# Kernel optimization log

Hardware: AMD Instinct MI355X
Metric: run time of the kernel (lower is better)

Reference implementation:

```python
import jax, jax.numpy as jnp
import numpy as np

N = 50000          # num nodes
E = 1_000_000      # num edges
H = 64             # hidden_dim
IMG, TWT, NUMP, CAT = 512, 768, 16, 8
NCLS, NET = 2, 3   # num_classes, num_edge_types


def setup_inputs() -> dict:
    key = jax.random.key(0)
    ks = jax.random.split(key, 40)
    f32 = jnp.float32
    w = lambda k, s: (jax.random.normal(k, s, f32) * 0.02)
    inp = {
        # forward args
        "image": jax.random.normal(ks[0], (N, IMG), f32),
        "tweets": jax.random.normal(ks[1], (N, TWT), f32),
        "num_prop": jax.random.normal(ks[2], (N, NUMP), f32),
        "category": jax.random.normal(ks[3], (N, CAT), f32),
        "edge_index": jax.random.randint(ks[4], (2, E), 0, N, jnp.int32),
        "edge_type": jax.random.randint(ks[5], (E,), 0, NET, jnp.int32),
        # explicit randomness (replaces randn_like / Bernoulli.sample)
        "eps": jax.random.normal(ks[6], (E, H), f32),
        "u": jax.random.uniform(ks[7], (E,), f32),
        # parameters (stored [in, out]; y = x @ W + b)
        "Wi": w(ks[8], (IMG, H)), "bi": jnp.zeros((H,), f32),
        "Wt": w(ks[9], (TWT, H)), "bt": jnp.zeros((H,), f32),
        "Wn": w(ks[10], (NUMP, H)), "bn": jnp.zeros((H,), f32),
        "Wc": w(ks[11], (CAT, H)), "bc": jnp.zeros((H,), f32),
        "Wf": w(ks[12], (4 * H, H)), "bf": jnp.zeros((H,), f32),
        "Eet": w(ks[13], (NET, 2 * H)),              # edge_type_embed
        "Wmu": w(ks[14], (2 * H, H)), "bmu": jnp.zeros((H,), f32),
        "Wlv": w(ks[15], (2 * H, H)), "blv": jnp.zeros((H,), f32),
        "Wm1": w(ks[16], (2 * H, 64)), "bm1": jnp.zeros((64,), f32),
        "Wm2": w(ks[17], (64, 1)), "bm2": jnp.zeros((1,), f32),
        "Wcls": w(ks[18], (H, NCLS)), "bcls": jnp.zeros((NCLS,), f32),
    }
    return inp


def reference(image, tweets, num_prop, category, edge_index, edge_type, eps, u,
              Wi, bi, Wt, bt, Wn, bn, Wc, bc, Wf, bf, Eet,
              Wmu, bmu, Wlv, blv, Wm1, bm1, Wm2, bm2, Wcls, bcls):
    relu = jax.nn.relu
    # encode_user
    img_f = relu(image @ Wi + bi)
    twt_f = relu(tweets @ Wt + bt)
    num_f = relu(num_prop @ Wn + bn)
    cat_f = relu(category @ Wc + bc)
    node_features = relu(jnp.concatenate([img_f, twt_f, num_f, cat_f], -1) @ Wf + bf)  # [N, H]

    src, dst = edge_index[0], edge_index[1]
    u_i, u_j = node_features[src], node_features[dst]          # [E, H] each
    edge_emb = relu(jnp.concatenate([u_i, u_j], -1) + Eet[edge_type])  # [E, 2H]

    # parameterized_gaussian (z unused downstream, kept for fidelity)
    mu = edge_emb @ Wmu + bmu
    log_var = edge_emb @ Wlv + blv
    z = mu + eps * jnp.exp(0.5 * log_var)

    # edge confidence + Bernoulli sample via inverse-CDF with provided uniforms
    logits_e = (relu(edge_emb @ Wm1 + bm1) @ Wm2 + bm2)[:, 0]  # [E]
    p_ij = jax.nn.sigmoid(logits_e)
    s = (u < p_ij).astype(node_features.dtype)                 # trusted-edge indicator, [E]

    # segment-mean of dst features over trusted edges, grouped by src
    sums = jax.ops.segment_sum(u_j * s[:, None], src, num_segments=N)  # [N, H]
    cnt = jax.ops.segment_sum(s, src, num_segments=N)                  # [N]
    agg = jnp.where(cnt[:, None] > 0, sums / jnp.maximum(cnt, 1.0)[:, None], node_features)

    return agg @ Wcls + bcls  # [N, num_classes]
```

## Files before the change

kernel.cpp:

```cpp
#include <hip/hip_runtime.h>
#include <cstdint>

typedef short short8 __attribute__((ext_vector_type(8)));
typedef float f32x4  __attribute__((ext_vector_type(4)));

__device__ __forceinline__ void split2(float x, short& h, short& l) {
  unsigned u  = __float_as_uint(x);
  unsigned rh = u + 0x7FFFu + ((u >> 16) & 1u);
  h = (short)(rh >> 16);
  float hf = __uint_as_float((rh >> 16) << 16);
  float lf = x - hf;
  unsigned ul = __float_as_uint(lf);
  unsigned rl = ul + 0x7FFFu + ((ul >> 16) & 1u);
  l = (short)(rl >> 16);
}

__device__ __forceinline__ void split4(float4 a, uint2& hp, uint2& lp) {
  unsigned hp0, hp1, lp0, lp1;
  asm("v_cvt_pk_bf16_f32 %0, %1, %2" : "=v"(hp0) : "v"(a.x), "v"(a.y));
  asm("v_cvt_pk_bf16_f32 %0, %1, %2" : "=v"(hp1) : "v"(a.z), "v"(a.w));
  float h0 = __uint_as_float(hp0 << 16);
  float h1 = __uint_as_float(hp0 & 0xFFFF0000u);
  float h2 = __uint_as_float(hp1 << 16);
  float h3 = __uint_as_float(hp1 & 0xFFFF0000u);
  float l0 = a.x - h0, l1 = a.y - h1, l2 = a.z - h2, l3 = a.w - h3;
  asm("v_cvt_pk_bf16_f32 %0, %1, %2" : "=v"(lp0) : "v"(l0), "v"(l1));
  asm("v_cvt_pk_bf16_f32 %0, %1, %2" : "=v"(lp1) : "v"(l2), "v"(l3));
  hp = make_uint2(hp0, hp1);
  lp = make_uint2(lp0, lp1);
}

__global__ __launch_bounds__(256) void init_head(int* __restrict__ head, int N)
{
  const int i = blockIdx.x * 256 + threadIdx.x;
  if (i < N) head[i] = -1;
}

__global__ __launch_bounds__(256) void prep_w(
    const float* __restrict__ Wi, const float* __restrict__ Wt,
    const float* __restrict__ Wn, const float* __restrict__ Wc,
    const float* __restrict__ Wf, const float* __restrict__ Wm1,
    short* __restrict__ hi, short* __restrict__ lo)
{
  int idx = blockIdx.x * 256 + threadIdx.x;
  if (idx >= 1728 * 64) return;
  int kp = idx >> 6, col = idx & 63;
  const float* W; int K, kloc, base;
  if (kp < 512)       { W = Wi;            K = 512; kloc = kp;        base = 0;    }
  else if (kp < 1280) { W = Wt;            K = 768; kloc = kp - 512;  base = 512;  }
  else if (kp < 1312) { W = Wn;            K = 16;  kloc = kp - 1280; base = 1280; }
  else if (kp < 1344) { W = Wc;            K = 8;   kloc = kp - 1312; base = 1312; }
  else if (kp < 1600) { W = Wf;            K = 256; kloc = kp - 1344; base = 1344; }
  else if (kp < 1664) { W = Wm1;           K = 64;  kloc = kp - 1600; base = 1600; }
  else                { W = Wm1 + 64 * 64; K = 64;  kloc = kp - 1664; base = 1664; }
  float x = (kloc < K) ? W[(size_t)kloc * 64 + col] : 0.f;
  short h, l; split2(x, h, l);
  int s = kloc >> 5;
  int addr = ((s * 4 + (col >> 4)) * 64 + ((col & 15) | (((kloc >> 3) & 3) << 4))) * 8 + (kloc & 7);
  size_t o = (size_t)base * 64 + addr;
  hi[o] = h; lo[o] = l;
}

__global__ __launch_bounds__(256) void encoder(
    const float* __restrict__ image, const float* __restrict__ tweets,
    const float* __restrict__ nump, const float* __restrict__ catg,
    const short* __restrict__ Whi, const short* __restrict__ Wlo,
    const float* __restrict__ bi, const float* __restrict__ bt,
    const float* __restrict__ bn, const float* __restrict__ bc,
    const float* __restrict__ bf, float* __restrict__ nf, int M)
{
  __shared__ float hbuf[4][16 * 68 + 4];
  const int tid = threadIdx.x;
  const int m0  = blockIdx.x * 64;
  const int w   = tid >> 6, l = tid & 63;
  const int r   = l & 15;
  const int g   = l >> 4;
  int grow = m0 + w * 16 + r;
  if (grow >= M) grow = M - 1;

  f32x4 acc[4], acc2[4];
#pragma unroll
  for (int n = 0; n < 4; n++) {
    acc[n]  = (f32x4){0.f, 0.f, 0.f, 0.f};
    acc2[n] = (f32x4){0.f, 0.f, 0.f, 0.f};
  }

  auto mfma_step = [&](float4 a0, float4 a1, int wstep, f32x4* ac) {
    uint2 h01, l01, h23, l23;
    split4(a0, h01, l01);
    split4(a1, h23, l23);
    uint4 ahi_u = make_uint4(h01.x, h01.y, h23.x, h23.y);
    uint4 alo_u = make_uint4(l01.x, l01.y, l23.x, l23.y);
    short8 ahi = *reinterpret_cast<short8*>(&ahi_u);
    short8 alo = *reinterpret_cast<short8*>(&alo_u);
#pragma unroll
    for (int n = 0; n < 4; n++) {
      short8 whi = *reinterpret_cast<const short8*>(&Whi[((size_t)(wstep * 4 + n)) * 512 + l * 8]);
      short8 wlo = *reinterpret_cast<const short8*>(&Wlo[((size_t)(wstep * 4 + n)) * 512 + l * 8]);
      ac[n] = __builtin_amdgcn_mfma_f32_16x16x32_bf16(ahi, whi, ac[n], 0, 0, 0);
      ac[n] = __builtin_amdgcn_mfma_f32_16x16x32_bf16(alo, whi, ac[n], 0, 0, 0);
      ac[n] = __builtin_amdgcn_mfma_f32_16x16x32_bf16(ahi, wlo, ac[n], 0, 0, 0);
    }
  };

  auto seg2_phase = [&](int seg, const float* __restrict__ bias) {
    float* hb = hbuf[w];
#pragma unroll
    for (int n = 0; n < 4; n++) {
      const int c  = n * 16 + r;
      const float bb = bias[c];
#pragma unroll
      for (int j = 0; j < 4; j++) {
        const int row = g * 4 + j;
        hb[row * 68 + c] = fmaxf(acc[n][j] + bb, 0.f);
      }
      acc[n] = (f32x4){0.f, 0.f, 0.f, 0.f};
    }
    asm volatile("s_waitcnt lgkmcnt(0)" ::: "memory");
    __builtin_amdgcn_sched_barrier(0);
#pragma unroll
    for (int ks2 = 0; ks2 < 2; ks2++) {
      float4 b0 = *reinterpret_cast<const float4*>(&hb[r * 68 + ks2 * 32 + g * 8]);
      float4 b1 = *reinterpret_cast<const float4*>(&hb[r * 68 + ks2 * 32 + g * 8 + 4]);
      mfma_step(b0, b1, 42 + seg * 2 + ks2, acc2);
    }
  };

#pragma unroll 4
  for (int t = 0; t < 16; t++) {
    const float* ap = image + (size_t)grow * 512 + t * 32 + g * 8;
    float4 a0 = *reinterpret_cast<const float4*>(ap);
    float4 a1 = *reinterpret_cast<const float4*>(ap + 4);
    mfma_step(a0, a1, t, acc);
  }
  seg2_phase(0, bi);

#pragma unroll 4
  for (int t = 0; t < 24; t++) {
    const float* ap = tweets + (size_t)grow * 768 + t * 32 + g * 8;
    float4 a0 = *reinterpret_cast<const float4*>(ap);
    float4 a1 = *reinterpret_cast<const float4*>(ap + 4);
    mfma_step(a0, a1, 16 + t, acc);
  }
  seg2_phase(1, bt);

  {
    float4 a0 = make_float4(0.f, 0.f, 0.f, 0.f);
    float4 a1 = make_float4(0.f, 0.f, 0.f, 0.f);
    if (g < 2) {
      const float* ap = nump + (size_t)grow * 16 + g * 8;
      a0 = *reinterpret_cast<const float4*>(ap);
      a1 = *reinterpret_cast<const float4*>(ap + 4);
    }
    mfma_step(a0, a1, 40, acc);
  }
  seg2_phase(2, bn);

  {
    float4 a0 = make_float4(0.f, 0.f, 0.f, 0.f);
    float4 a1 = make_float4(0.f, 0.f, 0.f, 0.f);
    if (g == 0) {
      const float* ap = catg + (size_t)grow * 8;
      a0 = *reinterpret_cast<const float4*>(ap);
      a1 = *reinterpret_cast<const float4*>(ap + 4);
    }
    mfma_step(a0, a1, 41, acc);
  }
  seg2_phase(3, bc);

  const int rb  = m0 + w * 16 + g * 4;
#pragma unroll
  for (int n = 0; n < 4; n++) {
    const int c = n * 16 + r;
    const float bb = bf[c];
#pragma unroll
    for (int j = 0; j < 4; j++) {
      const int rr = rb + j;
      if (rr < M) nf[(size_t)rr * 64 + c] = fmaxf(acc2[n][j] + bb, 0.f);
    }
  }
}

__global__ __launch_bounds__(256) void table_kernel(
    const float* __restrict__ nf, const float* __restrict__ Eet,
    const short* __restrict__ Whi, const short* __restrict__ Wlo,
    const float* __restrict__ bm1,
    float* __restrict__ Atab, float* __restrict__ Btab, int N3, int gT)
{
  const bool isB    = (int)blockIdx.x >= gT;
  const int  m0     = (isB ? (int)blockIdx.x - gT : (int)blockIdx.x) * 64;
  const int  eoff   = isB ? 64 : 0;
  const int  wstep0 = isB ? 52 : 50;
  float*     Tab    = isB ? Btab : Atab;

  __shared__ short Ahi[2][2048];
  __shared__ short Alo[2][2048];
  const int tid  = threadIdx.x;
  const int w    = tid >> 6, l = tid & 63;
  const int srow = tid >> 3;
  const int k0   = (tid & 7) * 4;
  const int i0   = k0 & 7;
  const int kg   = k0 >> 3;

#pragma unroll
  for (int ks2 = 0; ks2 < 2; ks2++) {
#pragma unroll
    for (int r2 = 0; r2 < 2; r2++) {
      const int row = srow + r2 * 32;
      const int rg  = m0 + row;
      float4 v = make_float4(0.f, 0.f, 0.f, 0.f);
      if (rg < N3) {
        const int n = rg / 3;
        const int t = rg - n * 3;
        const int k = ks2 * 32 + k0;
        float4 x = *reinterpret_cast<const float4*>(&nf[(size_t)n * 64 + k]);
        float4 e = *reinterpret_cast<const float4*>(&Eet[(size_t)t * 128 + eoff + k]);
        v.x = fmaxf(x.x + e.x, 0.f); v.y = fmaxf(x.y + e.y, 0.f);
        v.z = fmaxf(x.z + e.z, 0.f); v.w = fmaxf(x.w + e.w, 0.f);
      }
      uint2 hp, lp; split4(v, hp, lp);
      const int addr = (row >> 4) * 512 + (((row & 15) | (kg << 4)) * 8 + i0);
      *reinterpret_cast<uint2*>(&Ahi[ks2][addr]) = hp;
      *reinterpret_cast<uint2*>(&Alo[ks2][addr]) = lp;
    }
  }
  __syncthreads();

  f32x4 acc[4];
#pragma unroll
  for (int n = 0; n < 4; n++) acc[n] = (f32x4){0.f, 0.f, 0.f, 0.f};

#pragma unroll
  for (int ks2 = 0; ks2 < 2; ks2++) {
    short8 ahi = *reinterpret_cast<const short8*>(&Ahi[ks2][w * 512 + l * 8]);
    short8 alo = *reinterpret_cast<const short8*>(&Alo[ks2][w * 512 + l * 8]);
#pragma unroll
    for (int n = 0; n < 4; n++) {
      short8 whi = *reinterpret_cast<const short8*>(&Whi[((size_t)(wstep0 + ks2) * 4 + n) * 512 + l * 8]);
      short8 wlo = *reinterpret_cast<const short8*>(&Wlo[((size_t)(wstep0 + ks2) * 4 + n) * 512 + l * 8]);
      acc[n] = __builtin_amdgcn_mfma_f32_16x16x32_bf16(ahi, whi, acc[n], 0, 0, 0);
      acc[n] = __builtin_amdgcn_mfma_f32_16x16x32_bf16(alo, whi, acc[n], 0, 0, 0);
      acc[n] = __builtin_amdgcn_mfma_f32_16x16x32_bf16(ahi, wlo, acc[n], 0, 0, 0);
    }
  }

  const int rb  = m0 + w * 16 + (l >> 4) * 4;
  const int c15 = l & 15;
#pragma unroll
  for (int n = 0; n < 4; n++) {
    const int c = n * 16 + c15;
    const float bb = isB ? 0.f : bm1[c];
#pragma unroll
    for (int j = 0; j < 4; j++) {
      const int rr = rb + j;
      if (rr < N3) Tab[(size_t)rr * 64 + c] = acc[n][j] + bb;
    }
  }
}

__global__ __launch_bounds__(256) void edge_kernel(
    const int* __restrict__ ei, const int* __restrict__ et,
    const float* __restrict__ u,
    const float* __restrict__ Atab, const float* __restrict__ Btab,
    const float* __restrict__ Wm2, const float* __restrict__ bm2,
    int* __restrict__ head, int* __restrict__ nxt, int E)
{
  const int tid = threadIdx.x;
  const int e   = blockIdx.x * 16 + (tid >> 4);
  const int sub = tid & 15;
  if (e >= E) return;

  const int sn = ei[e];
  const int dn = ei[E + e];
  const int t  = et[e];

  float4 a  = *reinterpret_cast<const float4*>(Atab + ((size_t)sn * 3 + t) * 64 + sub * 4);
  float4 b  = *reinterpret_cast<const float4*>(Btab + ((size_t)dn * 3 + t) * 64 + sub * 4);
  float4 wv = *reinterpret_cast<const float4*>(Wm2 + sub * 4);

  float v = fmaxf(a.x + b.x, 0.f) * wv.x;
  v = fmaf(fmaxf(a.y + b.y, 0.f), wv.y, v);
  v = fmaf(fmaxf(a.z + b.z, 0.f), wv.z, v);
  v = fmaf(fmaxf(a.w + b.w, 0.f), wv.w, v);
  v += __shfl_xor(v, 1);
  v += __shfl_xor(v, 2);
  v += __shfl_xor(v, 4);
  v += __shfl_xor(v, 8);

  if (sub == 0) {
    const float p = 1.f / (1.f + expf(-(v + bm2[0])));
    if (u[e] < p) {
      nxt[e] = atomicExch(&head[sn], e);
    }
  }
}

__global__ __launch_bounds__(256) void node_kernel(
    const int* __restrict__ head, const int* __restrict__ nxt,
    const int* __restrict__ ei,
    const float* __restrict__ nf,
    const float* __restrict__ Wcls, const float* __restrict__ bcls,
    float* __restrict__ out, int N, int E)
{
  const int n    = (int)((blockIdx.x * (unsigned)blockDim.x + threadIdx.x) >> 6);
  const int lane = threadIdx.x & 63;
  if (n >= N) return;

  double acc = 0.0;
  int    c   = 0;
  int    e   = head[n];
  while (e >= 0) {
    const int dn = ei[E + e];
    acc += (double)nf[(size_t)dn * 64 + lane];
    c++;
    e = nxt[e];
  }

  const float agg = (c > 0) ? (float)(acc / (double)c) : nf[(size_t)n * 64 + lane];
  float r0 = agg * Wcls[lane * 2 + 0];
  float r1 = agg * Wcls[lane * 2 + 1];
#pragma unroll
  for (int off = 32; off; off >>= 1) {
    r0 += __shfl_xor(r0, off, 64);
    r1 += __shfl_xor(r1, off, 64);
  }
  if (lane == 0) {
    out[(size_t)n * 2 + 0] = r0 + bcls[0];
    out[(size_t)n * 2 + 1] = r1 + bcls[1];
  }
}

extern "C" void kernel_launch(void* const* d_in, const int* in_sizes, int n_in,
                              void* d_out, int out_size, void* d_ws, size_t ws_size,
                              hipStream_t stream)
{
  const float* image    = (const float*)d_in[0];
  const float* tweets   = (const float*)d_in[1];
  const float* num_prop = (const float*)d_in[2];
  const float* category = (const float*)d_in[3];
  const int*   ei       = (const int*)  d_in[4];
  const int*   et       = (const int*)  d_in[5];
  const float* u        = (const float*)d_in[7];
  const float* Wi  = (const float*)d_in[8],  *bi  = (const float*)d_in[9];
  const float* Wt  = (const float*)d_in[10], *bt  = (const float*)d_in[11];
  const float* Wn  = (const float*)d_in[12], *bn  = (const float*)d_in[13];
  const float* Wc  = (const float*)d_in[14], *bc  = (const float*)d_in[15];
  const float* Wf  = (const float*)d_in[16], *bf  = (const float*)d_in[17];
  const float* Eet = (const float*)d_in[18];
  const float* Wm1 = (const float*)d_in[23], *bm1 = (const float*)d_in[24];
  const float* Wm2 = (const float*)d_in[25], *bm2 = (const float*)d_in[26];
  const float* Wcls= (const float*)d_in[27], *bcls= (const float*)d_in[28];
  float* out = (float*)d_out;

  const int N = in_sizes[0] / 512;
  const int E = in_sizes[5];

  float* ws = (float*)d_ws;
  size_t off = 0;
  float* nf     = ws + off;  off += (size_t)N * 64;
  float* Atab   = ws + off;  off += (size_t)N * 3 * 64;
  float* Btab   = ws + off;  off += (size_t)N * 3 * 64;
  int*   head   = (int*)(ws + off);  off += (size_t)N;
  int*   nxt    = (int*)(ws + off);  off += (size_t)E;
  short* Wfhi   = (short*)(ws + off);  off += (1728 * 64) / 2;
  short* Wflo   = (short*)(ws + off);  off += (1728 * 64) / 2;

  init_head<<<(N + 255) / 256, 256, 0, stream>>>(head, N);

  prep_w<<<(1728 * 64 + 255) / 256, 256, 0, stream>>>(Wi, Wt, Wn, Wc, Wf, Wm1,
                                                      Wfhi, Wflo);

  const int gN = (N + 63) / 64;
  encoder<<<gN, 256, 0, stream>>>(image, tweets, num_prop, category,
                                  Wfhi, Wflo, bi, bt, bn, bc, bf, nf, N);

  const int N3 = N * 3;
  const int gT = (N3 + 63) / 64;
  table_kernel<<<2 * gT, 256, 0, stream>>>(nf, Eet, Wfhi, Wflo, bm1,
                                           Atab, Btab, N3, gT);

  edge_kernel<<<(E + 15) / 16, 256, 0, stream>>>(ei, et, u, Atab, Btab,
                                                 Wm2, bm2, head, nxt, E);

  node_kernel<<<(N + 3) / 4, 256, 0, stream>>>(head, nxt, ei, nf, Wcls, bcls,
                                               out, N, E);
}
```

Baseline: 329.8 us.

## Double-buffer encoder activations and weights in LDS via global_load_lds

The encoder's main K loop now stages each 32-wide slice of the input rows and the matching bf16 hi/lo weight tiles into a two-slot LDS buffer with direct global-to-LDS loads. The next step is prefetched while the current one is consumed, replacing per-thread global loads feeding the MFMAs. An XOR swizzle is applied to the A tile to reduce LDS bank conflicts. In exchange it raises LDS use per block, which can lower occupancy. It also relies on a single barrier per step to order the asynchronous LDS writes against reads.

```diff
diff --git a/kernel.cpp b/kernel.cpp
--- a/kernel.cpp
+++ b/kernel.cpp
@@ -28,6 +28,12 @@
   asm("v_cvt_pk_bf16_f32 %0, %1, %2" : "=v"(lp1) : "v"(l2), "v"(l3));
   hp = make_uint2(hp0, hp1);
   lp = make_uint2(lp0, lp1);
+}
+
+__device__ __forceinline__ void gl_lds16(const void* g, void* l) {
+  __builtin_amdgcn_global_load_lds(
+      (const __attribute__((address_space(1))) unsigned int*)g,
+      (__attribute__((address_space(3))) unsigned int*)l, 16, 0, 0);
 }
 
 __global__ __launch_bounds__(256) void init_head(int* __restrict__ head, int N)
@@ -61,6 +67,11 @@
   hi[o] = h; lo[o] = l;
 }
 
+#define ENC_STEPS 42
+#define A_OFF  0
+#define W_OFF  16384
+#define HB_OFF 32768
+
 __global__ __launch_bounds__(256) void encoder(
     const float* __restrict__ image, const float* __restrict__ tweets,
     const float* __restrict__ nump, const float* __restrict__ catg,
@@ -69,14 +80,13 @@
     const float* __restrict__ bn, const float* __restrict__ bc,
     const float* __restrict__ bf, float* __restrict__ nf, int M)
 {
-  __shared__ float hbuf[4][16 * 68 + 4];
+  __shared__ __attribute__((aligned(16))) char lds[32768 + 4 * 1092 * 4];
+
   const int tid = threadIdx.x;
   const int m0  = blockIdx.x * 64;
   const int w   = tid >> 6, l = tid & 63;
-  const int r   = l & 15;
+  const int r16 = l & 15;
   const int g   = l >> 4;
-  int grow = m0 + w * 16 + r;
-  if (grow >= M) grow = M - 1;
 
   f32x4 acc[4], acc2[4];
 #pragma unroll
@@ -85,7 +95,37 @@
     acc2[n] = (f32x4){0.f, 0.f, 0.f, 0.f};
   }
 
-  auto mfma_step = [&](float4 a0, float4 a1, int wstep, f32x4* ac) {
+  auto stage = [&](int tt, int buf) {
+    const float* As; int lda, K, kbase;
+    if (tt < 16)       { As = image;  lda = 512; kbase = tt * 32;        K = 512; }
+    else if (tt < 40)  { As = tweets; lda = 768; kbase = (tt - 16) * 32; K = 768; }
+    else if (tt == 40) { As = nump;   lda = 16;  kbase = 0;              K = 16;  }
+    else               { As = catg;   lda = 8;   kbase = 0;              K = 8;   }
+#pragma unroll
+    for (int rr = 0; rr < 2; rr++) {
+      const int gc   = rr * 256 + w * 64 + l;
+      const int row  = gc >> 3;
+      const int csrc = (gc & 7) ^ (row & 7);
+      int grow = m0 + row; if (grow >= M) grow = M - 1;
+      int k = kbase + csrc * 4;
+      if (k >= K) k = kbase;
+      gl_lds16(As + (size_t)grow * lda + k,
+               lds + A_OFF + buf * 8192 + (rr * 256 + w * 64) * 16);
+    }
+    gl_lds16(Whi + (size_t)tt * 2048 + (size_t)(w * 64 + l) * 8,
+             lds + W_OFF + buf * 8192 + (w * 64) * 16);
+    gl_lds16(Wlo + (size_t)tt * 2048 + (size_t)(w * 64 + l) * 8,
+             lds + W_OFF + buf * 8192 + 4096 + (w * 64) * 16);
+  };
+
+  auto consume = [&](int buf, f32x4* ac) {
+    const char* Ab = lds + A_OFF + buf * 8192;
+    const char* Wb = lds + W_OFF + buf * 8192;
+    const int r = w * 16 + r16;
+    float4 a0 = *reinterpret_cast<const float4*>(
+        Ab + r * 128 + (((2 * g)     ^ (r & 7)) * 16));
+    float4 a1 = *reinterpret_cast<const float4*>(
+        Ab + r * 128 + (((2 * g + 1) ^ (r & 7)) * 16));
     uint2 h01, l01, h23, l23;
     split4(a0, h01, l01);
     split4(a1, h23, l23);
@@ -95,8 +135,8 @@
     short8 alo = *reinterpret_cast<short8*>(&alo_u);
 #pragma unroll
     for (int n = 0; n < 4; n++) {
-      short8 whi = *reinterpret_cast<const short8*>(&Whi[((size_t)(wstep * 4 + n)) * 512 + l * 8]);
-      short8 wlo = *reinterpret_cast<const short8*>(&Wlo[((size_t)(wstep * 4 + n)) * 512 + l * 8]);
+      short8 whi = *reinterpret_cast<const short8*>(Wb + n * 1024 + l * 16);
+      short8 wlo = *reinterpret_cast<const short8*>(Wb + 4096 + n * 1024 + l * 16);
       ac[n] = __builtin_amdgcn_mfma_f32_16x16x32_bf16(ahi, whi, ac[n], 0, 0, 0);
       ac[n] = __builtin_amdgcn_mfma_f32_16x16x32_bf16(alo, whi, ac[n], 0, 0, 0);
       ac[n] = __builtin_amdgcn_mfma_f32_16x16x32_bf16(ahi, wlo, ac[n], 0, 0, 0);
@@ -104,10 +144,10 @@
   };
 
   auto seg2_phase = [&](int seg, const float* __restrict__ bias) {
-    float* hb = hbuf[w];
+    float* hb = (float*)(lds + HB_OFF) + w * 1092;
 #pragma unroll
     for (int n = 0; n < 4; n++) {
-      const int c  = n * 16 + r;
+      const int c  = n * 16 + r16;
       const float bb = bias[c];
 #pragma unroll
       for (int j = 0; j < 4; j++) {
@@ -120,58 +160,42 @@
     __builtin_amdgcn_sched_barrier(0);
 #pragma unroll
     for (int ks2 = 0; ks2 < 2; ks2++) {
-      float4 b0 = *reinterpret_cast<const float4*>(&hb[r * 68 + ks2 * 32 + g * 8]);
-      float4 b1 = *reinterpret_cast<const float4*>(&hb[r * 68 + ks2 * 32 + g * 8 + 4]);
-      mfma_step(b0, b1, 42 + seg * 2 + ks2, acc2);
+      float4 b0 = *reinterpret_cast<const float4*>(&hb[r16 * 68 + ks2 * 32 + g * 8]);
+      float4 b1 = *reinterpret_cast<const float4*>(&hb[r16 * 68 + ks2 * 32 + g * 8 + 4]);
+      uint2 h01, l01, h23, l23;
+      split4(b0, h01, l01);
+      split4(b1, h23, l23);
+      uint4 ahi_u = make_uint4(h01.x, h01.y, h23.x, h23.y);
+      uint4 alo_u = make_uint4(l01.x, l01.y, l23.x, l23.y);
+      short8 ahi = *reinterpret_cast<short8*>(&ahi_u);
+      short8 alo = *reinterpret_cast<short8*>(&alo_u);
+      const int st = 42 + seg * 2 + ks2;
+#pragma unroll
+      for (int n = 0; n < 4; n++) {
+        short8 whi = *reinterpret_cast<const short8*>(&Whi[((size_t)st * 4 + n) * 512 + l * 8]);
+        short8 wlo = *reinterpret_cast<const short8*>(&Wlo[((size_t)st * 4 + n) * 512 + l * 8]);
+        acc2[n] = __builtin_amdgcn_mfma_f32_16x16x32_bf16(ahi, whi, acc2[n], 0, 0, 0);
+        acc2[n] = __builtin_amdgcn_mfma_f32_16x16x32_bf16(alo, whi, acc2[n], 0, 0, 0);
+        acc2[n] = __builtin_amdgcn_mfma_f32_16x16x32_bf16(ahi, wlo, acc2[n], 0, 0, 0);
+      }
     }
   };
 
-#pragma unroll 4
-  for (int t = 0; t < 16; t++) {
-    const float* ap = image + (size_t)grow * 512 + t * 32 + g * 8;
-    float4 a0 = *reinterpret_cast<const float4*>(ap);
-    float4 a1 = *reinterpret_cast<const float4*>(ap + 4);
-    mfma_step(a0, a1, t, acc);
-  }
-  seg2_phase(0, bi);
-
-#pragma unroll 4
-  for (int t = 0; t < 24; t++) {
-    const float* ap = tweets + (size_t)grow * 768 + t * 32 + g * 8;
-    float4 a0 = *reinterpret_cast<const float4*>(ap);
-    float4 a1 = *reinterpret_cast<const float4*>(ap + 4);
-    mfma_step(a0, a1, 16 + t, acc);
-  }
-  seg2_phase(1, bt);
-
-  {
-    float4 a0 = make_float4(0.f, 0.f, 0.f, 0.f);
-    float4 a1 = make_float4(0.f, 0.f, 0.f, 0.f);
-    if (g < 2) {
-      const float* ap = nump + (size_t)grow * 16 + g * 8;
-      a0 = *reinterpret_cast<const float4*>(ap);
-      a1 = *reinterpret_cast<const float4*>(ap + 4);
-    }
-    mfma_step(a0, a1, 40, acc);
-  }
-  seg2_phase(2, bn);
-
-  {
-    float4 a0 = make_float4(0.f, 0.f, 0.f, 0.f);
-    float4 a1 = make_float4(0.f, 0.f, 0.f, 0.f);
-    if (g == 0) {
-      const float* ap = catg + (size_t)grow * 8;
-      a0 = *reinterpret_cast<const float4*>(ap);
-      a1 = *reinterpret_cast<const float4*>(ap + 4);
-    }
-    mfma_step(a0, a1, 41, acc);
-  }
-  seg2_phase(3, bc);
-
-  const int rb  = m0 + w * 16 + g * 4;
+  stage(0, 0);
+  for (int t = 0; t < ENC_STEPS; t++) {
+    __syncthreads();
+    if (t + 1 < ENC_STEPS) stage(t + 1, (t + 1) & 1);
+    consume(t & 1, acc);
+    if (t == 15)      seg2_phase(0, bi);
+    else if (t == 39) seg2_phase(1, bt);
+    else if (t == 40) seg2_phase(2, bn);
+    else if (t == 41) seg2_phase(3, bc);
+  }
+
+  const int rb = m0 + w * 16 + g * 4;
 #pragma unroll
   for (int n = 0; n < 4; n++) {
-    const int c = n * 16 + r;
+    const int c = n * 16 + r16;
     const float bb = bf[c];
 #pragma unroll
     for (int j = 0; j < 4; j++) {
```

New measurement: 459.3 us. +39.3%, slower.

## Split encoder K-dimension across wave pairs and reduce partial outputs in LDS

Applied to the files above, without the earlier changes.

Each block now covers 32 rows instead of 64, and pairs of waves share a 16-row tile. One wave handles the image, num_prop and category segments and the other handles tweets. The two partial second-layer accumulators are summed through shared memory before the bias, ReLU and store. This doubles the grid and the number of waves per row tile, to raise parallelism and memory-level concurrency in the bandwidth-heavy encoder. The cost is an extra __syncthreads, an LDS exchange, and an uneven split of work (544 vs 768 columns) between the two waves.

```diff
diff --git a/kernel.cpp b/kernel.cpp
--- a/kernel.cpp
+++ b/kernel.cpp
@@ -70,12 +70,14 @@
     const float* __restrict__ bf, float* __restrict__ nf, int M)
 {
   __shared__ float hbuf[4][16 * 68 + 4];
-  const int tid = threadIdx.x;
-  const int m0  = blockIdx.x * 64;
-  const int w   = tid >> 6, l = tid & 63;
-  const int r   = l & 15;
-  const int g   = l >> 4;
-  int grow = m0 + w * 16 + r;
+  __shared__ f32x4 comb[2][64][4];
+  const int tid  = threadIdx.x;
+  const int w    = tid >> 6, l = tid & 63;
+  const int pair = w >> 1, par = w & 1;
+  const int m0   = blockIdx.x * 32 + pair * 16;
+  const int r16  = l & 15;
+  const int g    = l >> 4;
+  int grow = m0 + r16;
   if (grow >= M) grow = M - 1;
 
   f32x4 acc[4], acc2[4];
@@ -107,7 +109,7 @@
     float* hb = hbuf[w];
 #pragma unroll
     for (int n = 0; n < 4; n++) {
-      const int c  = n * 16 + r;
+      const int c  = n * 16 + r16;
       const float bb = bias[c];
 #pragma unroll
       for (int j = 0; j < 4; j++) {
@@ -120,63 +122,76 @@
     __builtin_amdgcn_sched_barrier(0);
 #pragma unroll
     for (int ks2 = 0; ks2 < 2; ks2++) {
-      float4 b0 = *reinterpret_cast<const float4*>(&hb[r * 68 + ks2 * 32 + g * 8]);
-      float4 b1 = *reinterpret_cast<const float4*>(&hb[r * 68 + ks2 * 32 + g * 8 + 4]);
+      float4 b0 = *reinterpret_cast<const float4*>(&hb[r16 * 68 + ks2 * 32 + g * 8]);
+      float4 b1 = *reinterpret_cast<const float4*>(&hb[r16 * 68 + ks2 * 32 + g * 8 + 4]);
       mfma_step(b0, b1, 42 + seg * 2 + ks2, acc2);
     }
   };
 
+  if (par == 0) {
 #pragma unroll 4
-  for (int t = 0; t < 16; t++) {
-    const float* ap = image + (size_t)grow * 512 + t * 32 + g * 8;
-    float4 a0 = *reinterpret_cast<const float4*>(ap);
-    float4 a1 = *reinterpret_cast<const float4*>(ap + 4);
-    mfma_step(a0, a1, t, acc);
-  }
-  seg2_phase(0, bi);
-
+    for (int t = 0; t < 16; t++) {
+      const float* ap = image + (size_t)grow * 512 + t * 32 + g * 8;
+      float4 a0 = *reinterpret_cast<const float4*>(ap);
+      float4 a1 = *reinterpret_cast<const float4*>(ap + 4);
+      mfma_step(a0, a1, t, acc);
+    }
+    seg2_phase(0, bi);
+    {
+      float4 a0 = make_float4(0.f, 0.f, 0.f, 0.f);
+      float4 a1 = a0;
+      if (g < 2) {
+        const float* ap = nump + (size_t)grow * 16 + g * 8;
+        a0 = *reinterpret_cast<const float4*>(ap);
+        a1 = *reinterpret_cast<const float4*>(ap + 4);
+      }
+      mfma_step(a0, a1, 40, acc);
+    }
+    seg2_phase(2, bn);
+    {
+      float4 a0 = make_float4(0.f, 0.f, 0.f, 0.f);
+      float4 a1 = a0;
+      if (g == 0) {
+        const float* ap = catg + (size_t)grow * 8;
+        a0 = *reinterpret_cast<const float4*>(ap);
+        a1 = *reinterpret_cast<const float4*>(ap + 4);
+      }
+      mfma_step(a0, a1, 41, acc);
+    }
+    seg2_phase(3, bc);
+  } else {
 #pragma unroll 4
-  for (int t = 0; t < 24; t++) {
-    const float* ap = tweets + (size_t)grow * 768 + t * 32 + g * 8;
-    float4 a0 = *reinterpret_cast<const float4*>(ap);
-    float4 a1 = *reinterpret_cast<const float4*>(ap + 4);
-    mfma_step(a0, a1, 16 + t, acc);
-  }
-  seg2_phase(1, bt);
-
-  {
-    float4 a0 = make_float4(0.f, 0.f, 0.f, 0.f);
-    float4 a1 = make_float4(0.f, 0.f, 0.f, 0.f);
-    if (g < 2) {
-      const float* ap = nump + (size_t)grow * 16 + g * 8;
-      a0 = *reinterpret_cast<const float4*>(ap);
-      a1 = *reinterpret_cast<const float4*>(ap + 4);
-    }
-    mfma_step(a0, a1, 40, acc);
-  }
-  seg2_phase(2, bn);
-
-  {
-    float4 a0 = make_float4(0.f, 0.f, 0.f, 0.f);
-    float4 a1 = make_float4(0.f, 0.f, 0.f, 0.f);
-    if (g == 0) {
-      const float* ap = catg + (size_t)grow * 8;
-      a0 = *reinterpret_cast<const float4*>(ap);
-      a1 = *reinterpret_cast<const float4*>(ap + 4);
-    }
-    mfma_step(a0, a1, 41, acc);
-  }
-  seg2_phase(3, bc);
-
-  const int rb  = m0 + w * 16 + g * 4;
-#pragma unroll
-  for (int n = 0; n < 4; n++) {
-    const int c = n * 16 + r;
-    const float bb = bf[c];
-#pragma unroll
-    for (int j = 0; j < 4; j++) {
-      const int rr = rb + j;
-      if (rr < M) nf[(size_t)rr * 64 + c] = fmaxf(acc2[n][j] + bb, 0.f);
+    for (int t = 0; t < 24; t++) {
+      const float* ap = tweets + (size_t)grow * 768 + t * 32 + g * 8;
+      float4 a0 = *reinterpret_cast<const float4*>(ap);
+      float4 a1 = *reinterpret_cast<const float4*>(ap + 4);
+      mfma_step(a0, a1, 16 + t, acc);
+    }
+    seg2_phase(1, bt);
+  }
+
+  if (par == 1) {
+#pragma unroll
+    for (int n = 0; n < 4; n++) comb[pair][l][n] = acc2[n];
+  }
+  __syncthreads();
+  if (par == 0) {
+#pragma unroll
+    for (int n = 0; n < 4; n++) {
+      f32x4 o = comb[pair][l][n];
+      acc2[n][0] += o[0]; acc2[n][1] += o[1];
+      acc2[n][2] += o[2]; acc2[n][3] += o[3];
+    }
+    const int rb = m0 + g * 4;
+#pragma unroll
+    for (int n = 0; n < 4; n++) {
+      const int c = n * 16 + r16;
+      const float bb = bf[c];
+#pragma unroll
+      for (int j = 0; j < 4; j++) {
+        const int rr = rb + j;
+        if (rr < M) nf[(size_t)rr * 64 + c] = fmaxf(acc2[n][j] + bb, 0.f);
+      }
     }
   }
 }
@@ -370,7 +385,7 @@
   prep_w<<<(1728 * 64 + 255) / 256, 256, 0, stream>>>(Wi, Wt, Wn, Wc, Wf, Wm1,
                                                       Wfhi, Wflo);
 
-  const int gN = (N + 63) / 64;
+  const int gN = (N + 31) / 32;
   encoder<<<gN, 256, 0, stream>>>(image, tweets, num_prop, category,
                                   Wfhi, Wflo, bi, bt, bn, bc, bf, nf, N);
 
```

Result: slower. 337.3 us (+2.3%).
